# Optimization experiments

Hardware: AMD Instinct MI355X
Metric: run time of the kernel (lower is better)

Reference implementation:

```python
import jax, jax.numpy as jnp
import numpy as np

WS = 8  # window/grid size, hard-coded in GlobalCirculationBlock
NH = 8  # num_heads


def _ln(x, w, b):
    m = jnp.mean(x, -1, keepdims=True)
    v = jnp.mean((x - m) ** 2, -1, keepdims=True)
    return (x - m) * jax.lax.rsqrt(v + 1e-5) * w + b


def _attn(q, k, v, scale):
    # q,k,v: [..., S, hd]
    s = jnp.einsum('...qd,...kd->...qk', q, k) * scale
    return jnp.einsum('...qk,...kd->...qd', jax.nn.softmax(s, axis=-1), v)


def setup_inputs() -> dict:
    key = jax.random.key(0)
    ks = jax.random.split(key, 8)
    B, C, H, W = 8, 128, 128, 128
    hid = 4 * C
    f = lambda k, shape, s=0.02: jax.random.normal(k, shape, jnp.float32) * s
    z = lambda n: jnp.zeros((n,), jnp.float32)
    return {
        'x': f(ks[0], (B, C, H, W), 1.0),
        'conv_w': f(ks[1], (C, 1, 3, 3)),        # depthwise 3x3 pos embed
        'conv_b': z(C),
        'norm1_w': jnp.ones((C,), jnp.float32), 'norm1_b': z(C),
        'wqkv': f(ks[2], (C, 3 * C)),            # qkv_bias=False
        'proj_w': f(ks[3], (C, C)), 'proj_b': z(C),
        'norm2_w': jnp.ones((C,), jnp.float32), 'norm2_b': z(C),
        'fc1_w': f(ks[4], (C, hid)), 'fc1_b': z(hid),
        'fc2_w': f(ks[5], (hid, C)), 'fc2_b': z(C),
        'ls1': jnp.full((C,), 1e-2, jnp.float32),
        'ls2': jnp.full((C,), 1e-2, jnp.float32),
    }


def reference(x, conv_w, conv_b, norm1_w, norm1_b, wqkv, proj_w, proj_b,
              norm2_w, norm2_b, fc1_w, fc1_b, fc2_w, fc2_b, ls1, ls2):
    B, C, H, W = x.shape
    nh, ws = NH, WS
    hd = C // nh
    scale = hd ** -0.5
    nhl = nh // 2                     # local heads == global heads
    nH, nW = H // ws, W // ws         # H,W multiples of ws -> no padding

    # depthwise conv positional embedding + residual
    pos = jax.lax.conv_general_dilated(
        x, conv_w, (1, 1), 'SAME',
        dimension_numbers=('NCHW', 'OIHW', 'NCHW'), feature_group_count=C)
    x = x + pos + conv_b[None, :, None, None]

    xt = x.reshape(B, C, H * W).transpose(0, 2, 1)   # [B, N, C]

    # ---- dual-scale attention ----
    xn = _ln(xt, norm1_w, norm1_b).reshape(B, H, W, C)
    qkv = (xn @ wqkv).reshape(B, H, W, 3, nh, hd)
    q, k, v = qkv[:, :, :, 0], qkv[:, :, :, 1], qkv[:, :, :, 2]  # [B,H,W,nh,hd]

    # local branch: first nhl heads, window attention (seq = ws*ws)
    def win(t):  # [B,H,W,nhl,hd] -> [B,nH,nW,nhl,ws*ws,hd]
        t = t.reshape(B, nH, ws, nW, ws, nhl, hd)
        return t.transpose(0, 1, 3, 5, 2, 4, 6).reshape(B, nH, nW, nhl, ws * ws, hd)

    ol = _attn(win(q[..., :nhl, :]), win(k[..., :nhl, :]), win(v[..., :nhl, :]), scale)
    ol = (ol.reshape(B, nH, nW, nhl, ws, ws, hd)
            .transpose(0, 1, 4, 2, 5, 3, 6)
            .reshape(B, H, W, nhl * hd))

    # global branch: last nhl heads, grid attention (seq = nH*nW)
    def grd(t):  # [B,H,W,nhl,hd] -> [B,ws,ws,nhl,nH*nW,hd]
        t = t.reshape(B, nH, ws, nW, ws, nhl, hd)
        return t.transpose(0, 2, 4, 5, 1, 3, 6).reshape(B, ws, ws, nhl, nH * nW, hd)

    og = _attn(grd(q[..., nhl:, :]), grd(k[..., nhl:, :]), grd(v[..., nhl:, :]), scale)
    og = (og.reshape(B, ws, ws, nhl, nH, nW, hd)
            .transpose(0, 4, 1, 5, 2, 3, 6)
            .reshape(B, H, W, nhl * hd))

    a = jnp.concatenate([ol, og], axis=-1).reshape(B, H * W, C)
    a = a @ proj_w + proj_b
    xt = xt + ls1 * a

    # ---- MLP ----
    h = _ln(xt, norm2_w, norm2_b)
    h = jax.nn.gelu(h @ fc1_w + fc1_b, approximate=False) @ fc2_w + fc2_b
    xt = xt + ls2 * h

    return xt.transpose(0, 2, 1).reshape(B, C, H, W)
```

## Files before the change

### kernel.cpp

```cpp
#include <hip/hip_runtime.h>
#include <hip/hip_bf16.h>

typedef __hip_bfloat16 bf16;
typedef __attribute__((ext_vector_type(8))) short short8;
typedef __attribute__((ext_vector_type(4))) short short4v;
typedef __attribute__((ext_vector_type(4))) float floatx4;
typedef __attribute__((ext_vector_type(16))) float floatx16;

#define Bn 8
#define Cc 128
#define Hh 128
#define Wl 128
#define HW (Hh*Wl)
#define NT (Bn*HW)
#define REG 8388608

#define QSCALE 0.36067376022224085f
#if __has_builtin(__builtin_amdgcn_exp2f)
#define EXP2(x) __builtin_amdgcn_exp2f(x)
#else
#define EXP2(x) __expf((x)*0.69314718055994531f)
#endif

__device__ __forceinline__ float b2f(bf16 v){ return __bfloat162float(v); }
__device__ __forceinline__ bf16  f2b(float v){ return __float2bfloat16(v); }

#define GL16(gp, lp) __builtin_amdgcn_global_load_lds( \
    (__attribute__((address_space(1))) unsigned int*)(gp), \
    (__attribute__((address_space(3))) unsigned int*)(lp), 16, 0, 0)

__global__ __launch_bounds__(256) void transpose_all(const float* __restrict__ wqkv,
                                                     const float* __restrict__ proj_w,
                                                     const float* __restrict__ fc1_w,
                                                     const float* __restrict__ fc2_w,
                                                     bf16* __restrict__ qkvT,
                                                     bf16* __restrict__ projT,
                                                     bf16* __restrict__ fc1T,
                                                     bf16* __restrict__ fc2T){
  int idx = blockIdx.x*256 + threadIdx.x;
  const float* src; bf16* dst; int K, N;
  if(idx < 49152){ src=wqkv; dst=qkvT; K=128; N=384; }
  else if(idx < 65536){ idx -= 49152; src=proj_w; dst=projT; K=128; N=128; }
  else if(idx < 131072){ idx -= 65536; src=fc1_w; dst=fc1T; K=128; N=512; }
  else { idx -= 131072; src=fc2_w; dst=fc2T; K=512; N=128; }
  int n = idx % N, k = idx / N;
  dst[(size_t)n*K + k] = f2b(src[idx]);
}

__global__ __launch_bounds__(256) void conv_kernel(const float* __restrict__ x,
                                                   const float* __restrict__ cw,
                                                   const float* __restrict__ cb,
                                                   float* __restrict__ xt){
  __shared__ float tile[16][132];
  int blk = blockIdx.x;
  int h = blk & 127; int t = blk >> 7;
  int cg = t & 7;    int b = t >> 3;
  int w4 = threadIdx.x & 31;
  int ci = threadIdx.x >> 5;
  int w0 = w4*4;
#pragma unroll
  for(int cc=0; cc<2; cc++){
    int c = cg*16 + ci*2 + cc;
    const float* xp = x + ((size_t)(b*Cc + c))*HW;
    float wg[9];
#pragma unroll
    for(int i=0;i<9;i++) wg[i] = cw[c*9+i];
    float4 rowv[3]; float lf[3], rt[3];
#pragma unroll
    for(int r=0;r<3;r++){
      int hh = h-1+r;
      float4 v = {0.f,0.f,0.f,0.f};
      if(hh>=0 && hh<Hh) v = *(const float4*)(xp + hh*Wl + w0);
      rowv[r] = v;
      float l = __shfl_up(v.w, 1, 32);
      float rr = __shfl_down(v.x, 1, 32);
      lf[r] = (w4==0)  ? 0.f : l;
      rt[r] = (w4==31) ? 0.f : rr;
    }
    float acc0 = cb[c], acc1 = cb[c], acc2 = cb[c], acc3 = cb[c];
#pragma unroll
    for(int r=0;r<3;r++){
      float4 v = rowv[r];
      acc0 += wg[r*3+0]*lf[r] + wg[r*3+1]*v.x + wg[r*3+2]*v.y;
      acc1 += wg[r*3+0]*v.x   + wg[r*3+1]*v.y + wg[r*3+2]*v.z;
      acc2 += wg[r*3+0]*v.y   + wg[r*3+1]*v.z + wg[r*3+2]*v.w;
      acc3 += wg[r*3+0]*v.z   + wg[r*3+1]*v.w + wg[r*3+2]*rt[r];
    }
    acc0 += rowv[1].x; acc1 += rowv[1].y; acc2 += rowv[1].z; acc3 += rowv[1].w;
    float4 o = {acc0, acc1, acc2, acc3};
    *(float4*)&tile[ci*2+cc][w0] = o;
  }
  __syncthreads();
  const size_t obase = ((size_t)b*HW + (size_t)h*Wl)*Cc + cg*16;
#pragma unroll
  for(int i=0;i<8;i++){
    int idx = i*256 + threadIdx.x;
    int c2 = idx & 15, w2 = idx >> 4;
    xt[obase + (size_t)w2*Cc + c2] = tile[c2][w2];
  }
}

__global__ __launch_bounds__(256) void ln_kernel(const float* __restrict__ xt,
                                                 const float* __restrict__ wv,
                                                 const float* __restrict__ bv,
                                                 bf16* __restrict__ xn){
  int tok  = blockIdx.x*4 + (threadIdx.x>>6);
  int lane = threadIdx.x & 63;
  const float* row = xt + (size_t)tok*Cc;
  float v0 = row[lane], v1 = row[lane+64];
  float s = v0+v1;
#pragma unroll
  for(int off=32; off; off>>=1) s += __shfl_down(s, off, 64);
  s = __shfl(s, 0, 64);
  float m = s * (1.0f/128.0f);
  float d0 = v0-m, d1 = v1-m;
  float vs = d0*d0 + d1*d1;
#pragma unroll
  for(int off=32; off; off>>=1) vs += __shfl_down(vs, off, 64);
  vs = __shfl(vs, 0, 64);
  float rstd = rsqrtf(vs*(1.0f/128.0f) + 1e-5f);
  bf16* orow = xn + (size_t)tok*Cc;
  orow[lane]    = f2b(d0*rstd*wv[lane]    + bv[lane]);
  orow[lane+64] = f2b(d1*rstd*wv[lane+64] + bv[lane+64]);
}

template<int EPI>
__global__ __launch_bounds__(256) void mfma_gemm(const bf16* __restrict__ A,
                                                 const bf16* __restrict__ Wt,
                                                 const float* __restrict__ bias,
                                                 bf16* __restrict__ outb,
                                                 float* __restrict__ xt,
                                                 const float* __restrict__ ls,
                                                 int N, int K){
  __shared__ short As[2][128*32];
  __shared__ short Bs[2][64*32];
  const int tid  = threadIdx.x;
  const int lane = tid & 63;
  const int w    = tid >> 6;

  const int nwg = gridDim.x * gridDim.y;
  const int lin = blockIdx.y * gridDim.x + blockIdx.x;
  const int t   = (lin & 7) * (nwg >> 3) + (lin >> 3);
  const int m0  = (t / gridDim.x) * 128;
  const int n0  = (t % gridDim.x) * 64;

  const int l1 = tid + 256;
  const bf16* gA0 = A  + (size_t)(m0 + ((tid>>6)<<4) + (tid&15))*K + (((tid>>4)&3)<<3);
  const bf16* gA1 = A  + (size_t)(m0 + ((l1 >>6)<<4) + (l1 &15))*K + (((l1 >>4)&3)<<3);
  const bf16* gB  = Wt + (size_t)(n0 + ((tid>>6)<<4) + (tid&15))*K + (((tid>>4)&3)<<3);
  const int ldsA0 = w*512;
  const int ldsA1 = 2048 + w*512;
  const int ldsB  = w*512;

  floatx4 acc[4][2];
#pragma unroll
  for(int i=0;i<4;i++)
#pragma unroll
    for(int j=0;j<2;j++) acc[i][j] = (floatx4){0.f,0.f,0.f,0.f};

  const int nk = K >> 5;
  GL16(gA0, &As[0][ldsA0]);
  GL16(gA1, &As[0][ldsA1]);
  GL16(gB , &Bs[0][ldsB ]);
  __syncthreads();

  int cur = 0;
  for(int it=0; it<nk; ++it){
    if(it+1 < nk){
      const int kn = (it+1) << 5;
      GL16(gA0 + kn, &As[cur^1][ldsA0]);
      GL16(gA1 + kn, &As[cur^1][ldsA1]);
      GL16(gB  + kn, &Bs[cur^1][ldsB ]);
    }
    short8 af[4], bfr[2];
#pragma unroll
    for(int mt=0;mt<4;mt++) af[mt] = *(short8*)&As[cur][(((w&1)*4+mt)*64 + lane)*8];
#pragma unroll
    for(int nt=0;nt<2;nt++) bfr[nt] = *(short8*)&Bs[cur][(((w>>1)*2+nt)*64 + lane)*8];
#pragma unroll
    for(int mt=0;mt<4;mt++)
#pragma unroll
      for(int nt=0;nt<2;nt++)
        acc[mt][nt] = __builtin_amdgcn_mfma_f32_16x16x32_bf16(af[mt], bfr[nt], acc[mt][nt], 0, 0, 0);
    __syncthreads();
    cur ^= 1;
  }

#pragma unroll
  for(int mt=0;mt<4;mt++){
#pragma unroll
    for(int nt=0;nt<2;nt++){
#pragma unroll
      for(int r=0;r<4;r++){
        int row = m0 + (w&1)*64 + mt*16 + ((lane>>4))*4 + r;
        int col = n0 + (w>>1)*32 + nt*16 + (lane&15);
        float v = acc[mt][nt][r];
        if(EPI==0){
          int reg = col >> 6;
          int head = (col >> 4) & 3;
          int ch = col & 15;
          int b = row >> 14, h = (row >> 7) & 127, ww = row & 127;
          if(reg < 2) v *= QSCALE;
          size_t didx;
          if(!(reg & 1)){
            int inst = ((b*16 + (h>>3))*16 + (ww>>3))*4 + head;
            int pos = (h&7)*8 + (ww&7);
            didx = ((size_t)inst*64 + pos)*16 + ch;
          } else {
            int inst = ((b*8 + (h&7))*8 + (ww&7))*4 + head;
            int pos = (h>>3)*16 + (ww>>3);
            didx = ((size_t)inst*256 + pos)*16 + ch;
          }
          outb[(size_t)reg*REG + didx] = f2b(v);
        } else if(EPI==2){
          v += bias[col];
          xt[(size_t)row*128 + col] += ls[col]*v;
        }
      }
    }
  }
}

__global__ __launch_bounds__(256) void fused_mlp(const float* __restrict__ xt,
                                                 const bf16* __restrict__ W1,
                                                 const float* __restrict__ b1,
                                                 const bf16* __restrict__ W2,
                                                 const float* __restrict__ b2,
                                                 const float* __restrict__ nw,
                                                 const float* __restrict__ nb,
                                                 const float* __restrict__ ls,
                                                 float* __restrict__ out){
  extern __shared__ short lds[];
  const int W1OFF = 0, W2OFF = 8192, HSOFF = 16384;
  const int tid = threadIdx.x, lane = tid & 63, w = tid >> 6;
  const int n16 = lane & 15, quad = lane >> 4;
  const int lin = blockIdx.x;
  const int t = (lin & 7)*128 + (lin >> 3);
  const int mw = t*128 + w*32;

  auto stage = [&](int nc, int buf){
    const bf16* W1c = W1 + (size_t)nc*32*128;
#pragma unroll
    for(int p=0;p<2;p++){
      int fid = p*4 + w;
      int nt = fid >> 2, ks = fid & 3;
      GL16(W1c + (size_t)(nt*16 + n16)*128 + ks*32 + quad*8, &lds[W1OFF + buf*4096 + fid*512]);
      GL16(W2 + (size_t)(fid*16 + n16)*512 + nc*32 + quad*8, &lds[W2OFF + buf*4096 + fid*512]);
    }
  };

  stage(0, 0);

  float wreg[4][8], breg[4][8];
#pragma unroll
  for(int ks=0;ks<4;ks++){
    *(float4*)&wreg[ks][0] = *(const float4*)(nw + ks*32 + quad*8);
    *(float4*)&wreg[ks][4] = *(const float4*)(nw + ks*32 + quad*8 + 4);
    *(float4*)&breg[ks][0] = *(const float4*)(nb + ks*32 + quad*8);
    *(float4*)&breg[ks][4] = *(const float4*)(nb + ks*32 + quad*8 + 4);
  }
  short8 areg[2][4];
#pragma unroll
  for(int mt=0;mt<2;mt++){
    const float* xr = xt + (size_t)(mw + mt*16 + n16)*128;
    float av[4][8]; float s = 0.f, qs = 0.f;
#pragma unroll
    for(int ks=0;ks<4;ks++){
      *(float4*)&av[ks][0] = *(const float4*)(xr + ks*32 + quad*8);
      *(float4*)&av[ks][4] = *(const float4*)(xr + ks*32 + quad*8 + 4);
#pragma unroll
      for(int j=0;j<8;j++){ s += av[ks][j]; qs += av[ks][j]*av[ks][j]; }
    }
    s  += __shfl_xor(s, 16, 64);  s  += __shfl_xor(s, 32, 64);
    qs += __shfl_xor(qs, 16, 64); qs += __shfl_xor(qs, 32, 64);
    float m = s*(1.0f/128.0f);
    float rstd = rsqrtf(qs*(1.0f/128.0f) - m*m + 1e-5f);
#pragma unroll
    for(int ks=0;ks<4;ks++){
      short8 t8;
#pragma unroll
      for(int j=0;j<8;j++){
        bf16 g = f2b((av[ks][j]-m)*rstd*wreg[ks][j] + breg[ks][j]);
        ((short*)&t8)[j] = *(short*)&g;
      }
      areg[mt][ks] = t8;
    }
  }

  floatx4 acc2[2][8];
#pragma unroll
  for(int i=0;i<2;i++)
#pragma unroll
    for(int j=0;j<8;j++) acc2[i][j] = (floatx4){0.f,0.f,0.f,0.f};

  short* hw = &lds[HSOFF + w*1280];

  __syncthreads();

  for(int nc=0; nc<16; ++nc){
    const int cur = nc & 1;
    if(nc+1 < 16) stage(nc+1, cur^1);

    const short* W1b = &lds[W1OFF + cur*4096];
    floatx4 acc1[2][2];
#pragma unroll
    for(int i=0;i<2;i++)
#pragma unroll
      for(int j=0;j<2;j++) acc1[i][j] = (floatx4){0.f,0.f,0.f,0.f};
#pragma unroll
    for(int ks=0;ks<4;ks++){
#pragma unroll
      for(int nt=0;nt<2;nt++){
        short8 bfr = *(const short8*)&W1b[(nt*4+ks)*512 + lane*8];
#pragma unroll
        for(int mt=0;mt<2;mt++)
          acc1[mt][nt] = __builtin_amdgcn_mfma_f32_16x16x32_bf16(areg[mt][ks], bfr, acc1[mt][nt], 0, 0, 0);
      }
    }

#pragma unroll
    for(int nt=0;nt<2;nt++){
      float bb = b1[nc*32 + nt*16 + n16];
#pragma unroll
      for(int mt=0;mt<2;mt++){
#pragma unroll
        for(int r=0;r<4;r++){
          float v = acc1[mt][nt][r] + bb;
          float u = v*v;
          float e = EXP2(v*__fmaf_rn(u, 0.044715f, 1.0f)*(-2.3022127f));
          float g = v*__builtin_amdgcn_rcpf(1.0f + e);
          bf16 gb = f2b(g);
          hw[(mt*16 + quad*4 + r)*40 + nt*16 + n16] = *(short*)&gb;
        }
      }
    }

    const short* W2b = &lds[W2OFF + cur*4096];
    short8 ha[2];
#pragma unroll
    for(int mt=0;mt<2;mt++) ha[mt] = *(short8*)&hw[(mt*16 + n16)*40 + quad*8];
#pragma unroll
    for(int nt2=0;nt2<8;nt2++){
      short8 bf2 = *(const short8*)&W2b[nt2*512 + lane*8];
#pragma unroll
      for(int mt=0;mt<2;mt++)
        acc2[mt][nt2] = __builtin_amdgcn_mfma_f32_16x16x32_bf16(ha[mt], bf2, acc2[mt][nt2], 0, 0, 0);
    }

    __syncthreads();
  }

  const int t128 = t*128;
  const int bI = t128 >> 14;
  const int hw0 = t128 & (HW-1);
  float* op = out + (size_t)bI*Cc*HW + hw0;
  float* tlf = (float*)lds;
  const int cI = tid >> 4, toff = (tid & 15)*8;
#pragma unroll
  for(int nt2=0;nt2<8;nt2++){
    int col = nt2*16 + n16;
    float bb = b2[col], lsv = ls[col];
#pragma unroll
    for(int mt=0;mt<2;mt++){
#pragma unroll
      for(int r=0;r<4;r++){
        int row = mw + mt*16 + quad*4 + r;
        float v = acc2[mt][nt2][r] + bb;
        tlf[n16*132 + (w*32 + mt*16 + quad*4 + r)] = xt[(size_t)row*128 + col] + lsv*v;
      }
    }
    __syncthreads();
    float4 v0 = *(float4*)&tlf[cI*132 + toff];
    float4 v1 = *(float4*)&tlf[cI*132 + toff + 4];
    *(float4*)&op[(size_t)(nt2*16 + cI)*HW + toff]     = v0;
    *(float4*)&op[(size_t)(nt2*16 + cI)*HW + toff + 4] = v1;
    __syncthreads();
  }
}

__global__ __launch_bounds__(256) void attn_local2(const bf16* __restrict__ qL,
                                                   const bf16* __restrict__ kL,
                                                   const bf16* __restrict__ vL,
                                                   bf16* __restrict__ a){
  __shared__ short vt[16*72];
  __shared__ short pb[4][16*72];
  const int tid = threadIdx.x;
  const int w = tid >> 6, lane = tid & 63;
  const int n16 = lane & 15, quad = lane >> 4;
  const int blk = blockIdx.x;
  const int head = blk & 3, winid = blk >> 2;
  const bf16* Qb = qL + (size_t)blk*1024;
  const bf16* Kb = kL + (size_t)blk*1024;
  const bf16* Vb = vL + (size_t)blk*1024;

  if(tid < 128){
    int tok = tid >> 1, u = tid & 1;
    short8 v = *(const short8*)(Vb + tok*16 + u*8);
#pragma unroll
    for(int i=0;i<8;i++) vt[(u*8+i)*72 + tok] = ((short*)&v)[i];
  }
  __syncthreads();

  const int qt = w;
  short8 qf = {0,0,0,0,0,0,0,0};
  if(quad < 2) qf = *(const short8*)(Qb + (qt*16+n16)*16 + quad*8);

  floatx4 sf[4];
#pragma unroll
  for(int kt=0; kt<4; kt++){
    short8 kf = {0,0,0,0,0,0,0,0};
    if(quad < 2) kf = *(const short8*)(Kb + (kt*16+n16)*16 + quad*8);
    floatx4 z = (floatx4){0.f,0.f,0.f,0.f};
    sf[kt] = __builtin_amdgcn_mfma_f32_16x16x32_bf16(qf, kf, z, 0, 0, 0);
  }

  float mx[4] = {-1e30f,-1e30f,-1e30f,-1e30f};
#pragma unroll
  for(int kt=0; kt<4; kt++)
#pragma unroll
    for(int r=0;r<4;r++) mx[r] = fmaxf(mx[r], sf[kt][r]);
#pragma unroll
  for(int r=0;r<4;r++){
    mx[r] = fmaxf(mx[r], __shfl_xor(mx[r], 1, 64));
    mx[r] = fmaxf(mx[r], __shfl_xor(mx[r], 2, 64));
    mx[r] = fmaxf(mx[r], __shfl_xor(mx[r], 4, 64));
    mx[r] = fmaxf(mx[r], __shfl_xor(mx[r], 8, 64));
    mx[r] = -mx[r];
  }
  float l[4] = {0.f,0.f,0.f,0.f};
#pragma unroll
  for(int kt=0; kt<4; kt++){
#pragma unroll
    for(int r=0;r<4;r++){
      float p = EXP2(sf[kt][r] + mx[r]);
      l[r] += p;
      bf16 pbv = f2b(p);
      pb[w][(quad*4+r)*72 + kt*16 + n16] = *(short*)&pbv;
    }
  }
#pragma unroll
  for(int r=0;r<4;r++){
    l[r] += __shfl_xor(l[r], 1, 64);
    l[r] += __shfl_xor(l[r], 2, 64);
    l[r] += __shfl_xor(l[r], 4, 64);
    l[r] += __shfl_xor(l[r], 8, 64);
  }

  floatx4 of = (floatx4){0.f,0.f,0.f,0.f};
#pragma unroll
  for(int kb=0; kb<2; kb++){
    short8 pf = *(short8*)&pb[w][n16*72 + kb*32 + quad*8];
    short8 vfb = *(short8*)&vt[n16*72 + kb*32 + quad*8];
    of = __builtin_amdgcn_mfma_f32_16x16x32_bf16(pf, vfb, of, 0, 0, 0);
  }

  const int wj = winid & 15, wi = (winid >> 4) & 15, b = winid >> 8;
  const int ooff = head*16;
#pragma unroll
  for(int r=0;r<4;r++){
    int pos = qt*16 + quad*4 + r;
    int h = wi*8 + (pos>>3), ww = wj*8 + (pos&7);
    size_t t = (size_t)b*HW + (size_t)h*Wl + ww;
    a[t*Cc + ooff + n16] = f2b(of[r] / l[r]);
  }
}

__global__ __launch_bounds__(256) void attn_grid2(const bf16* __restrict__ qG,
                                                  const bf16* __restrict__ kG,
                                                  const bf16* __restrict__ vG,
                                                  bf16* __restrict__ a){
  __shared__ short vt[16*264];
  __shared__ short pb[4][32*136];
  const int tid = threadIdx.x;
  const int w = tid >> 6, lane = tid & 63;
  const int n16 = lane & 15, quad = lane >> 4;
  const int q32 = lane & 31, hb = lane >> 5;
  const int blk = blockIdx.x;
  const int head = blk & 3, ginst = blk >> 2;
  const bf16* Qb = qG + (size_t)blk*4096;
  const bf16* Kb = kG + (size_t)blk*4096;
  const bf16* Vb = vG + (size_t)blk*4096;

#pragma unroll
  for(int it=0; it<2; it++){
    int chunk = it*256 + tid;
    int tok = chunk >> 1, u = chunk & 1;
    short8 v = *(const short8*)(Vb + tok*16 + u*8);
#pragma unroll
    for(int i=0;i<8;i++) vt[(u*8+i)*264 + tok] = ((short*)&v)[i];
  }
  __syncthreads();

  const int sj = ginst & 7, si = (ginst >> 3) & 7, b = ginst >> 6;
  const int ooff = 64 + head*16;
  short* pbw = pb[w];
  const floatx16 Z16 = {0.f,0.f,0.f,0.f,0.f,0.f,0.f,0.f,0.f,0.f,0.f,0.f,0.f,0.f,0.f,0.f};

#pragma unroll
  for(int qi=0; qi<2; qi++){
    const int q0 = w*64 + qi*32;
    const short8 qf = *(const short8*)(Qb + (size_t)(q0 + q32)*16 + hb*8);
    float l_acc = 0.f;
    floatx4 of0 = (floatx4){0.f,0.f,0.f,0.f};
    floatx4 of1 = (floatx4){0.f,0.f,0.f,0.f};
#pragma unroll
    for(int kc=0; kc<2; kc++){
#pragma unroll
      for(int kt=0; kt<4; kt++){
        short8 kf = *(const short8*)(Kb + (size_t)(kc*128 + kt*32 + q32)*16 + hb*8);
        floatx16 s = __builtin_amdgcn_mfma_f32_32x32x16_bf16(kf, qf, Z16, 0, 0, 0);
#pragma unroll
        for(int g=0; g<4; g++){
          float p0 = EXP2(s[4*g+0]);
          float p1 = EXP2(s[4*g+1]);
          float p2 = EXP2(s[4*g+2]);
          float p3 = EXP2(s[4*g+3]);
          l_acc += (p0+p1)+(p2+p3);
          short4v pk = { (short)__bfloat16_as_ushort(f2b(p0)),
                         (short)__bfloat16_as_ushort(f2b(p1)),
                         (short)__bfloat16_as_ushort(f2b(p2)),
                         (short)__bfloat16_as_ushort(f2b(p3)) };
          *(short4v*)&pbw[q32*136 + kt*32 + g*8 + hb*4] = pk;
        }
      }
#pragma unroll
      for(int kb=0; kb<4; kb++){
        short8 vf  = *(short8*)&vt[n16*264 + kc*128 + kb*32 + quad*8];
        short8 pf0 = *(short8*)&pbw[n16*136 + kb*32 + quad*8];
        of0 = __builtin_amdgcn_mfma_f32_16x16x32_bf16(pf0, vf, of0, 0, 0, 0);
        short8 pf1 = *(short8*)&pbw[(16+n16)*136 + kb*32 + quad*8];
        of1 = __builtin_amdgcn_mfma_f32_16x16x32_bf16(pf1, vf, of1, 0, 0, 0);
      }
    }
    l_acc += __shfl_xor(l_acc, 32, 64);
#pragma unroll
    for(int hf=0; hf<2; hf++){
      floatx4 of = hf ? of1 : of0;
#pragma unroll
      for(int r=0;r<4;r++){
        float lr = __shfl(l_acc, hf*16 + quad*4 + r, 64);
        int pos = q0 + hf*16 + quad*4 + r;
        int h = (pos>>4)*8 + si, ww = (pos&15)*8 + sj;
        size_t t = (size_t)b*HW + (size_t)h*Wl + ww;
        a[t*Cc + ooff + n16] = f2b(of[r] / lr);
      }
    }
  }
}

extern "C" void kernel_launch(void* const* d_in, const int* in_sizes, int n_in,
                              void* d_out, int out_size, void* d_ws, size_t ws_size,
                              hipStream_t stream) {
  const float* x       = (const float*)d_in[0];
  const float* conv_w  = (const float*)d_in[1];
  const float* conv_b  = (const float*)d_in[2];
  const float* norm1_w = (const float*)d_in[3];
  const float* norm1_b = (const float*)d_in[4];
  const float* wqkv    = (const float*)d_in[5];
  const float* proj_w  = (const float*)d_in[6];
  const float* proj_b  = (const float*)d_in[7];
  const float* norm2_w = (const float*)d_in[8];
  const float* norm2_b = (const float*)d_in[9];
  const float* fc1_w   = (const float*)d_in[10];
  const float* fc1_b   = (const float*)d_in[11];
  const float* fc2_w   = (const float*)d_in[12];
  const float* fc2_b   = (const float*)d_in[13];
  const float* ls1     = (const float*)d_in[14];
  const float* ls2     = (const float*)d_in[15];
  float* out = (float*)d_out;

  char* ws = (char*)d_ws;
  float* xt = (float*)ws;
  bf16*  sh = (bf16*)(ws + (size_t)NT*Cc*4);
  bf16*  qh = (bf16*)(ws + (size_t)NT*Cc*4 + (size_t)NT*Cc*2);
  bf16*  wt = (bf16*)(ws + (size_t)NT*Cc*4 + (size_t)NT*Cc*2 + (size_t)NT*512*2);
  bf16* qkvT = wt;
  bf16* projT= wt + 49152;
  bf16* fc1T = wt + 65536;
  bf16* fc2T = wt + 131072;

  transpose_all<<<196608/256, 256, 0, stream>>>(wqkv, proj_w, fc1_w, fc2_w,
                                                qkvT, projT, fc1T, fc2T);
  conv_kernel<<<Bn*8*Hh, 256, 0, stream>>>(x, conv_w, conv_b, xt);
  ln_kernel<<<NT/4, 256, 0, stream>>>(xt, norm1_w, norm1_b, sh);
  mfma_gemm<0><<<dim3(384/64, NT/128), 256, 0, stream>>>(sh, qkvT, nullptr, qh, nullptr, nullptr, 384, 128);
  attn_grid2<<<2048, 256, 0, stream>>>(qh + (size_t)1*REG, qh + (size_t)3*REG, qh + (size_t)5*REG, sh);
  attn_local2<<<8192, 256, 0, stream>>>(qh + (size_t)0*REG, qh + (size_t)2*REG, qh + (size_t)4*REG, sh);
  mfma_gemm<2><<<dim3(128/64, NT/128), 256, 0, stream>>>(sh, projT, proj_b, nullptr, xt, ls1, 128, 128);
  fused_mlp<<<NT/128, 256, 43008, stream>>>(xt, fc1T, fc1_b, fc2T, fc2_b,
                                            norm2_w, norm2_b, ls2, out);
}
```

Measured before the change: 401.7 us.

## Fuse depthwise conv and first LayerNorm into one row-tile kernel

Merges the depthwise conv positional embedding and the norm1 LayerNorm into one kernel. Each block computes all 128 channels for one image row into a ~67 KB LDS tile, derives per-token mean and rstd, then writes both the fp32 residual and the bf16 normalized activations with vector stores. This removes the round trip of re-reading the fp32 xt buffer in a separate LN pass and one launch. In exchange it uses a large LDS footprint that lowers occupancy, a serial 128-iteration stats loop on half the threads, and a single-pass variance (E[x^2]-m^2) that is numerically less stable.

```diff
diff --git a/kernel.cpp b/kernel.cpp
--- a/kernel.cpp
+++ b/kernel.cpp
@@ -47,81 +47,91 @@
   dst[(size_t)n*K + k] = f2b(src[idx]);
 }
 
-__global__ __launch_bounds__(256) void conv_kernel(const float* __restrict__ x,
-                                                   const float* __restrict__ cw,
-                                                   const float* __restrict__ cb,
-                                                   float* __restrict__ xt){
-  __shared__ float tile[16][132];
-  int blk = blockIdx.x;
-  int h = blk & 127; int t = blk >> 7;
-  int cg = t & 7;    int b = t >> 3;
-  int w4 = threadIdx.x & 31;
-  int ci = threadIdx.x >> 5;
-  int w0 = w4*4;
-#pragma unroll
-  for(int cc=0; cc<2; cc++){
-    int c = cg*16 + ci*2 + cc;
-    const float* xp = x + ((size_t)(b*Cc + c))*HW;
-    float wg[9];
-#pragma unroll
-    for(int i=0;i<9;i++) wg[i] = cw[c*9+i];
-    float4 rowv[3]; float lf[3], rt[3];
-#pragma unroll
-    for(int r=0;r<3;r++){
-      int hh = h-1+r;
-      float4 v = {0.f,0.f,0.f,0.f};
-      if(hh>=0 && hh<Hh) v = *(const float4*)(xp + hh*Wl + w0);
-      rowv[r] = v;
-      float l = __shfl_up(v.w, 1, 32);
-      float rr = __shfl_down(v.x, 1, 32);
-      lf[r] = (w4==0)  ? 0.f : l;
-      rt[r] = (w4==31) ? 0.f : rr;
-    }
-    float acc0 = cb[c], acc1 = cb[c], acc2 = cb[c], acc3 = cb[c];
-#pragma unroll
-    for(int r=0;r<3;r++){
-      float4 v = rowv[r];
-      acc0 += wg[r*3+0]*lf[r] + wg[r*3+1]*v.x + wg[r*3+2]*v.y;
-      acc1 += wg[r*3+0]*v.x   + wg[r*3+1]*v.y + wg[r*3+2]*v.z;
-      acc2 += wg[r*3+0]*v.y   + wg[r*3+1]*v.z + wg[r*3+2]*v.w;
-      acc3 += wg[r*3+0]*v.z   + wg[r*3+1]*v.w + wg[r*3+2]*rt[r];
-    }
-    acc0 += rowv[1].x; acc1 += rowv[1].y; acc2 += rowv[1].z; acc3 += rowv[1].w;
-    float4 o = {acc0, acc1, acc2, acc3};
-    *(float4*)&tile[ci*2+cc][w0] = o;
+__global__ __launch_bounds__(256) void conv_ln_kernel(const float* __restrict__ x,
+                                                      const float* __restrict__ cw,
+                                                      const float* __restrict__ cb,
+                                                      const float* __restrict__ wv,
+                                                      const float* __restrict__ bv,
+                                                      float* __restrict__ xt,
+                                                      bf16* __restrict__ xn){
+  extern __shared__ float lds_f[];
+  float* tile = lds_f;
+  float* ms = lds_f + 128*132;
+  float* rs = ms + 128;
+  const int tid = threadIdx.x;
+  const int blk = blockIdx.x;
+  const int h = blk & 127, b = blk >> 7;
+  const int w4 = tid & 31;
+  const int ci = tid >> 5;
+  const int w0 = w4*4;
+
+  for(int cg=0; cg<8; cg++){
+#pragma unroll
+    for(int cc=0; cc<2; cc++){
+      int c = cg*16 + ci*2 + cc;
+      const float* xp = x + ((size_t)(b*Cc + c))*HW;
+      float wg[9];
+#pragma unroll
+      for(int i=0;i<9;i++) wg[i] = cw[c*9+i];
+      float4 rowv[3]; float lf[3], rt[3];
+#pragma unroll
+      for(int r=0;r<3;r++){
+        int hh = h-1+r;
+        float4 v = {0.f,0.f,0.f,0.f};
+        if(hh>=0 && hh<Hh) v = *(const float4*)(xp + hh*Wl + w0);
+        rowv[r] = v;
+        float l = __shfl_up(v.w, 1, 32);
+        float rr = __shfl_down(v.x, 1, 32);
+        lf[r] = (w4==0)  ? 0.f : l;
+        rt[r] = (w4==31) ? 0.f : rr;
+      }
+      float acc0 = cb[c], acc1 = cb[c], acc2 = cb[c], acc3 = cb[c];
+#pragma unroll
+      for(int r=0;r<3;r++){
+        float4 v = rowv[r];
+        acc0 += wg[r*3+0]*lf[r] + wg[r*3+1]*v.x + wg[r*3+2]*v.y;
+        acc1 += wg[r*3+0]*v.x   + wg[r*3+1]*v.y + wg[r*3+2]*v.z;
+        acc2 += wg[r*3+0]*v.y   + wg[r*3+1]*v.z + wg[r*3+2]*v.w;
+        acc3 += wg[r*3+0]*v.z   + wg[r*3+1]*v.w + wg[r*3+2]*rt[r];
+      }
+      acc0 += rowv[1].x; acc1 += rowv[1].y; acc2 += rowv[1].z; acc3 += rowv[1].w;
+      float4 o = {acc0, acc1, acc2, acc3};
+      *(float4*)&tile[c*132 + w0] = o;
+    }
   }
   __syncthreads();
-  const size_t obase = ((size_t)b*HW + (size_t)h*Wl)*Cc + cg*16;
-#pragma unroll
-  for(int i=0;i<8;i++){
-    int idx = i*256 + threadIdx.x;
-    int c2 = idx & 15, w2 = idx >> 4;
-    xt[obase + (size_t)w2*Cc + c2] = tile[c2][w2];
-  }
-}
-
-__global__ __launch_bounds__(256) void ln_kernel(const float* __restrict__ xt,
-                                                 const float* __restrict__ wv,
-                                                 const float* __restrict__ bv,
-                                                 bf16* __restrict__ xn){
-  int tok  = blockIdx.x*4 + (threadIdx.x>>6);
-  int lane = threadIdx.x & 63;
-  const float* row = xt + (size_t)tok*Cc;
-  float v0 = row[lane], v1 = row[lane+64];
-  float s = v0+v1;
-#pragma unroll
-  for(int off=32; off; off>>=1) s += __shfl_down(s, off, 64);
-  s = __shfl(s, 0, 64);
-  float m = s * (1.0f/128.0f);
-  float d0 = v0-m, d1 = v1-m;
-  float vs = d0*d0 + d1*d1;
-#pragma unroll
-  for(int off=32; off; off>>=1) vs += __shfl_down(vs, off, 64);
-  vs = __shfl(vs, 0, 64);
-  float rstd = rsqrtf(vs*(1.0f/128.0f) + 1e-5f);
-  bf16* orow = xn + (size_t)tok*Cc;
-  orow[lane]    = f2b(d0*rstd*wv[lane]    + bv[lane]);
-  orow[lane+64] = f2b(d1*rstd*wv[lane+64] + bv[lane+64]);
+
+  if(tid < 128){
+    float s = 0.f, qs = 0.f;
+    for(int c=0;c<128;c++){
+      float v = tile[c*132 + tid];
+      s += v; qs += v*v;
+    }
+    float m = s*(1.0f/128.0f);
+    ms[tid] = m;
+    rs[tid] = rsqrtf(qs*(1.0f/128.0f) - m*m + 1e-5f);
+  }
+  __syncthreads();
+
+  const int tok = tid >> 1, ch0 = (tid & 1)*64;
+  const float m = ms[tok], rstd = rs[tok];
+  const size_t base = ((size_t)b*HW + (size_t)h*Wl + tok)*Cc + ch0;
+#pragma unroll
+  for(int j0=0;j0<64;j0+=8){
+    short8 o8;
+    float xo[8];
+#pragma unroll
+    for(int j=0;j<8;j++){
+      int c = ch0 + j0 + j;
+      float v = tile[c*132 + tok];
+      xo[j] = v;
+      bf16 g = f2b((v-m)*rstd*wv[c] + bv[c]);
+      ((short*)&o8)[j] = *(short*)&g;
+    }
+    *(short8*)(xn + base + j0) = o8;
+    *(float4*)(xt + base + j0)     = *(float4*)&xo[0];
+    *(float4*)(xt + base + j0 + 4) = *(float4*)&xo[4];
+  }
 }
 
 template<int EPI>
@@ -581,8 +591,8 @@
 
   transpose_all<<<196608/256, 256, 0, stream>>>(wqkv, proj_w, fc1_w, fc2_w,
                                                 qkvT, projT, fc1T, fc2T);
-  conv_kernel<<<Bn*8*Hh, 256, 0, stream>>>(x, conv_w, conv_b, xt);
-  ln_kernel<<<NT/4, 256, 0, stream>>>(xt, norm1_w, norm1_b, sh);
+  conv_ln_kernel<<<Bn*Hh, 256, (128*132 + 256)*4, stream>>>(x, conv_w, conv_b,
+                                                            norm1_w, norm1_b, xt, sh);
   mfma_gemm<0><<<dim3(384/64, NT/128), 256, 0, stream>>>(sh, qkvT, nullptr, qh, nullptr, nullptr, 384, 128);
   attn_grid2<<<2048, 256, 0, stream>>>(qh + (size_t)1*REG, qh + (size_t)3*REG, qh + (size_t)5*REG, sh);
   attn_local2<<<8192, 256, 0, stream>>>(qh + (size_t)0*REG, qh + (size_t)2*REG, qh + (size_t)4*REG, sh);
```

New measurement: 444.8 us. 10.7% more time.
